# Kernel tuning notes

Hardware: AMD Instinct MI355X
Metric: run time of the kernel (lower is better)

The kernel has to match this reference:

```python
import jax, jax.numpy as jnp
import numpy as np

B, T, ENC_C = 64, 512, 512   # batch, encoder frames, encoder channels
H = 512                      # hidden_channels
D = 80                       # out_channels (mel dim)
RF = 2                       # reduction_factor
PRE_IN = D * RF              # prenet input (= D*2, see go_frame)
PRE_INNER = 256
CONV_CH = 32                 # location conv channels
K = 31                       # location conv kernel size


def setup_inputs():
    key = jax.random.key(0)
    ks = jax.random.split(key, 16)
    s = 0.02
    f32 = jnp.float32
    p = {}
    p['enc_output'] = jax.random.normal(ks[0], (B, T, ENC_C), f32)
    # acoustic lengths in [T, 2T], multiples of RF -> len//RF in [T//2, T]
    p['data_len'] = (jax.random.randint(ks[1], (B,), T // 2, T + 1, jnp.int32) * RF).astype(jnp.int32)
    # Prenet: two 1x1 convs (== linears) + ReLU
    p['pn_w1'] = jax.random.normal(ks[2], (PRE_INNER, PRE_IN), f32) * s
    p['pn_b1'] = jnp.zeros((PRE_INNER,), f32)
    p['pn_w2'] = jax.random.normal(ks[3], (H, PRE_INNER), f32) * s
    p['pn_b2'] = jnp.zeros((H,), f32)
    # Location-sensitive attention
    p['att_enc_w'] = jax.random.normal(ks[4], (H, ENC_C), f32) * s
    p['att_enc_b'] = jnp.zeros((H,), f32)
    p['att_dec_w'] = jax.random.normal(ks[5], (H, H), f32) * s
    p['att_conv_w'] = jax.random.normal(ks[6], (CONV_CH, 1, K), f32) * s
    p['att_loc_w'] = jax.random.normal(ks[7], (H, CONV_CH), f32) * s
    p['att_v_w'] = jax.random.normal(ks[8], (H,), f32) * s
    p['att_v_b'] = jnp.zeros((), f32)
    # 2 GRU cells (torch GRUCell layout: gates [r|z|n])
    p['gru0_wih'] = jax.random.normal(ks[9], (3 * H, ENC_C + H), f32) * s
    p['gru0_whh'] = jax.random.normal(ks[10], (3 * H, H), f32) * s
    p['gru0_bih'] = jnp.zeros((3 * H,), f32)
    p['gru0_bhh'] = jnp.zeros((3 * H,), f32)
    p['gru1_wih'] = jax.random.normal(ks[11], (3 * H, H), f32) * s
    p['gru1_whh'] = jax.random.normal(ks[12], (3 * H, H), f32) * s
    p['gru1_bih'] = jnp.zeros((3 * H,), f32)
    p['gru1_bhh'] = jnp.zeros((3 * H,), f32)
    # out_layer: 1x1 Conv1d(2H -> D*RF) == linear
    p['out_w'] = jax.random.normal(ks[13], (D * RF, 2 * H), f32) * s
    p['out_b'] = jnp.zeros((D * RF,), f32)
    return p


def _gru(x, h, wih, whh, bih, bhh):
    gi = x @ wih.T + bih
    gh = h @ whh.T + bhh
    ir, iz, inn = jnp.split(gi, 3, axis=-1)
    hr, hz, hn = jnp.split(gh, 3, axis=-1)
    r = jax.nn.sigmoid(ir + hr)
    z = jax.nn.sigmoid(iz + hz)
    n = jnp.tanh(inn + r * hn)
    return (1.0 - z) * n + z * h


def _decode(enc_output, data_len, pn_w1, pn_b1, pn_w2, pn_b2,
            att_enc_w, att_enc_b, att_dec_w, att_conv_w, att_loc_w, att_v_w, att_v_b,
            gru0_wih, gru0_whh, gru0_bih, gru0_bhh,
            gru1_wih, gru1_whh, gru1_bih, gru1_bhh, out_w, out_b):
    dt = enc_output.dtype
    len_r = data_len // RF                                   # (B,) encoder-frame lengths
    pad = jnp.arange(T)[None, :] >= len_r[:, None]           # (B,T) True at padding
    valid = (~pad).astype(dt)
    att_prev0 = valid / len_r.astype(dt)[:, None]            # uniform init attention
    # processed memory (computed once, as in attention.reset_state caching)
    pm = jnp.einsum('btc,hc->bth', enc_output, att_enc_w) + att_enc_b

    def step(carry, t):
        h0, h1, prev_out, att_sum = carry
        prev_w = jnp.where(t == 0, att_prev0, att_sum)       # (B,T)
        # location features: 1D conv over previous (cumulative) attention
        f = jax.lax.conv_general_dilated(prev_w[:, None, :], att_conv_w,
                                         (1,), [(K // 2, K // 2)])  # (B,CONV_CH,T)
        loc = jnp.einsum('bct,hc->bth', f, att_loc_w)
        dec = (h0 @ att_dec_w.T)[:, None, :]                 # query from GRU layer 0 state
        erg = jnp.tanh(loc + pm + dec) @ att_v_w + att_v_b   # (B,T)
        erg = jnp.where(pad, jnp.asarray(-1e9, dt), erg)
        att_w = jax.nn.softmax(erg, axis=-1)
        att_c = jnp.einsum('bt,btc->bc', att_w, enc_output)  # context (B,ENC_C)
        # prenet (dropout in eval == identity)
        x = jax.nn.relu(prev_out @ pn_w1.T + pn_b1)
        x = jax.nn.relu(x @ pn_w2.T + pn_b2)
        h0n = _gru(jnp.concatenate([x, att_c], -1), h0, gru0_wih, gru0_whh, gru0_bih, gru0_bhh)
        h1n = _gru(h0n, h1, gru1_wih, gru1_whh, gru1_bih, gru1_bhh)
        out = jnp.concatenate([h1n, att_c], -1) @ out_w.T + out_b   # (B, D*RF)
        return (h0n, h1n, out, att_sum + att_w), (out, att_w)

    zeros = lambda *s: jnp.zeros(s, dt)
    carry0 = (zeros(B, H), zeros(B, H), zeros(B, D * RF), zeros(B, T))
    _, (outs, att_ws) = jax.lax.scan(step, carry0, jnp.arange(T))
    # outs: (T,B,D*RF); each step reshapes to (B,D,RF) and cats on time
    out = outs.transpose(1, 0, 2).reshape(B, T, D, RF).transpose(0, 2, 1, 3).reshape(B, D, T * RF)
    att_w = att_ws.transpose(1, 2, 0)                        # (B, T, T_steps)
    return out, att_w


def reference(enc_output, data_len, pn_w1, pn_b1, pn_w2, pn_b2,
              att_enc_w, att_enc_b, att_dec_w, att_conv_w, att_loc_w, att_v_w, att_v_b,
              gru0_wih, gru0_whh, gru0_bih, gru0_bhh,
              gru1_wih, gru1_whh, gru1_bih, gru1_bhh, out_w, out_b):
    return _decode(enc_output, data_len, pn_w1, pn_b1, pn_w2, pn_b2,
                   att_enc_w, att_enc_b, att_dec_w, att_conv_w, att_loc_w, att_v_w, att_v_b,
                   gru0_wih, gru0_whh, gru0_bih, gru0_bhh,
                   gru1_wih, gru1_whh, gru1_bih, gru1_bhh, out_w, out_b)
```

## Files before the change

kernel.cpp:

```cpp
#include <hip/hip_runtime.h>
#include <hip/hip_bf16.h>

typedef unsigned short u16;


__device__ __forceinline__ float b2f(u16 u) {
  return __uint_as_float(((unsigned)u) << 16);
}
__device__ __forceinline__ u16 f2b(float f) {
  unsigned u = __float_as_uint(f);
  u += 0x7fffu + ((u >> 16) & 1u);
  return (u16)(u >> 16);
}
template<bool F32>
__device__ __forceinline__ float ldw(const void* p, size_t i) {
  return F32 ? ((const float*)p)[i] : b2f(((const u16*)p)[i]);
}
template<bool F32>
__device__ __forceinline__ float4 ldw4(const void* p, size_t i) {
  if (F32) {
    return *(const float4*)((const float*)p + i);
  } else {
    uint2 u = *(const uint2*)((const u16*)p + i);
    float4 r;
    r.x = __uint_as_float(u.x << 16);
    r.y = __uint_as_float(u.x & 0xffff0000u);
    r.z = __uint_as_float(u.y << 16);
    r.w = __uint_as_float(u.y & 0xffff0000u);
    return r;
  }
}
template<bool F32>
__device__ __forceinline__ void stout(void* p, size_t i, float v) {
  if (F32) ((float*)p)[i] = v; else ((u16*)p)[i] = f2b(v);
}
__device__ __forceinline__ float frcp(float x) { return __builtin_amdgcn_rcpf(x); }
__device__ __forceinline__ float tanh_f(float x) {
  float e = __expf(2.f * x);
  return 1.f - 2.f * frcp(e + 1.f);
}
__device__ __forceinline__ float sig_f(float x) { return frcp(1.f + __expf(-x)); }

__device__ __forceinline__ void st_sc(int* p, int v) {
  __hip_atomic_store(p, v, __ATOMIC_RELAXED, __HIP_MEMORY_SCOPE_AGENT);
}
__device__ __forceinline__ int ld_sc(const int* p) {
  return __hip_atomic_load(p, __ATOMIC_RELAXED, __HIP_MEMORY_SCOPE_AGENT);
}
__device__ __forceinline__ void stf_sc(float* p, float v) {
  __hip_atomic_store(p, v, __ATOMIC_RELAXED, __HIP_MEMORY_SCOPE_AGENT);
}
__device__ __forceinline__ float ldf_sc(const float* p) {
  return __hip_atomic_load(p, __ATOMIC_RELAXED, __HIP_MEMORY_SCOPE_AGENT);
}

__device__ __forceinline__ void stage_n(float* lds, const float* src, int n, int tid) {
  int i = 0;
  for (; i + 8192 <= n; i += 8192) {
    float r[16];
#pragma unroll
    for (int j = 0; j < 16; ++j) r[j] = ldf_sc(src + i + tid + j * 512);
#pragma unroll
    for (int j = 0; j < 16; ++j) lds[i + tid + j * 512] = r[j];
  }
  for (; i < n; i += 2048) {
    float r[4];
#pragma unroll
    for (int j = 0; j < 4; ++j) r[j] = ldf_sc(src + i + tid + j * 512);
#pragma unroll
    for (int j = 0; j < 4; ++j) lds[i + tid + j * 512] = r[j];
  }
}

template<bool F32, int NR>
__device__ __forceinline__ void dotN(float* __restrict__ acc, const float* __restrict__ sb,
                                     const void* __restrict__ wb, size_t rb, int wstride,
                                     int nk, int lane, int vz) {
  float4 wa[NR], wn[NR];
#pragma unroll
  for (int i = 0; i < NR; ++i) wa[i] = ldw4<F32>(wb, rb + (size_t)i * wstride + vz);
  for (int kg = 0; kg < nk; kg += 8) {
#pragma unroll
    for (int i = 0; i < NR; ++i) wn[i] = ldw4<F32>(wb, rb + (size_t)i * wstride + kg + 4 + vz);
    float a0 = sb[(kg + 0) * 64 + lane], a1 = sb[(kg + 1) * 64 + lane],
          a2 = sb[(kg + 2) * 64 + lane], a3 = sb[(kg + 3) * 64 + lane];
#pragma unroll
    for (int i = 0; i < NR; ++i)
      acc[i] = fmaf(wa[i].w, a3, fmaf(wa[i].z, a2, fmaf(wa[i].y, a1, fmaf(wa[i].x, a0, acc[i]))));
    int kn = (kg + 8 < nk) ? kg + 8 : kg;
#pragma unroll
    for (int i = 0; i < NR; ++i) wa[i] = ldw4<F32>(wb, rb + (size_t)i * wstride + kn + vz);
    float b0 = sb[(kg + 4) * 64 + lane], b1 = sb[(kg + 5) * 64 + lane],
          b2 = sb[(kg + 6) * 64 + lane], b3 = sb[(kg + 7) * 64 + lane];
#pragma unroll
    for (int i = 0; i < NR; ++i)
      acc[i] = fmaf(wn[i].w, b3, fmaf(wn[i].z, b2, fmaf(wn[i].y, b1, fmaf(wn[i].x, b0, acc[i]))));
  }
}

constexpr size_t OBAR  = 0;
constexpr size_t OFLG  = OBAR  + 128;
constexpr size_t OASUM = OFLG  + 8192;
constexpr size_t ODEC  = OASUM + 32768;
constexpr size_t OH0   = ODEC  + 32768;
constexpr size_t OH1   = OH0   + 32768;
constexpr size_t OPO   = OH1   + 32768;
constexpr size_t OZEND = OPO   + 10240;
constexpr int    ZERO_SPAN_N = (int)OZEND;
constexpr size_t OPRV  = OZEND;
constexpr size_t OERG  = OPRV  + 32768;
constexpr size_t OX1   = OERG  + 32768;
constexpr size_t OX2   = OX1   + 16384;
constexpr size_t OATTC = OX2   + 32768;
constexpr size_t OMM   = OATTC + 32768;
constexpr size_t OGI0  = OMM   + 16384;
constexpr size_t OGH0  = OGI0  + 393216;
constexpr size_t OGH1  = OGH0  + 196608;
constexpr size_t OGI1  = OGH1  + 196608;
constexpr size_t OPM   = OGI1  + 393216;
constexpr size_t OTOT  = OPM   + 8388608;

__device__ __forceinline__ void fastbar(int* flags, int* gen, int target,
                                        int wg, int tid) {
  __syncthreads();
  if (tid == 0) st_sc(flags + wg * 32, target);
  if (wg == 0) {
    if (tid < 64) {
      int i0 = tid * 4;
      for (;;) {
        int ok = (ld_sc(flags + (i0 + 0) * 32) >= target)
               & (ld_sc(flags + (i0 + 1) * 32) >= target)
               & (ld_sc(flags + (i0 + 2) * 32) >= target)
               & (ld_sc(flags + (i0 + 3) * 32) >= target);
        if (__ballot(ok) == 0xFFFFFFFFFFFFFFFFull) break;
      }
      if (tid == 0) st_sc(gen, target);
    }
    __syncthreads();
  } else {
    if (tid == 0) {
      while (ld_sc(gen) < target) {}
    }
    __syncthreads();
  }
}

__global__ void k_zero(float* p, int n) {
  for (int i = blockIdx.x * 256 + threadIdx.x; i < n; i += gridDim.x * 256) p[i] = 0.f;
}
__global__ void k_detect(int* flag, const u16* probe) {
  if (blockIdx.x != 0 || threadIdx.x != 0) return;
  int sane = 0;
  for (int i = 0; i < 256; i += 2) {
    u16 u = probe[i];
    int e = (u >> 7) & 0xFF;
    if (u == 0 || (e >= 97 && e <= 140)) ++sane;
  }
  *flag = (sane < 96) ? 1 : 0;
}
__global__ void k_prevw(float* prevw, const int* dlen) {
  int b = blockIdx.x;
  int len = dlen[b] >> 1;
  float inv = 1.f / (float)len;
  for (int i = threadIdx.x; i < 512; i += 256)
    prevw[b * 512 + i] = (i < len) ? inv : 0.f;
}
template<bool F32>
__global__ void k_cvtT512(const int* flag, float* dst, const void* src) {
  if (*flag != (F32 ? 1 : 0)) return;
  for (int i = blockIdx.x * 256 + threadIdx.x; i < 262144; i += gridDim.x * 256) {
    int c = i >> 9, h = i & 511;
    dst[i] = ldw<F32>(src, (size_t)h * 512 + c);
  }
}
template<bool F32>
__global__ void k_mmat(const int* flag, float* M, const void* locw, const void* convw) {
  if (*flag != (F32 ? 1 : 0)) return;
  int i = blockIdx.x * 256 + threadIdx.x;
  if (i >= 16384) return;
  int h = i >> 5, k = i & 31;
  float acc = 0.f;
  if (k < 31) {
    for (int c = 0; c < 32; ++c)
      acc = fmaf(ldw<F32>(locw, h * 32 + c), ldw<F32>(convw, c * 31 + k), acc);
  }
  M[i] = acc;
}
template<bool F32>
__global__ __launch_bounds__(256) void k_pm(const int* flag, u16* pm, const void* enc,
                                            const float* encwT, const void* encb) {
  if (*flag != (F32 ? 1 : 0)) return;
  __shared__ float encf[16 * 512];
  int row0 = blockIdx.x * 16;
  int tid = threadIdx.x;
  for (int i = tid; i < 16 * 512; i += 256) {
    int r = i >> 9, c = i & 511;
    encf[i] = ldw<F32>(enc, (size_t)(row0 + r) * 512 + c);
  }
  __syncthreads();
  float a0[16], a1[16];
  float bb0 = ldw<F32>(encb, tid), bb1 = ldw<F32>(encb, tid + 256);
#pragma unroll
  for (int r = 0; r < 16; ++r) { a0[r] = bb0; a1[r] = bb1; }
  for (int c = 0; c < 512; ++c) {
    float w0 = encwT[c * 512 + tid];
    float w1 = encwT[c * 512 + 256 + tid];
#pragma unroll
    for (int r = 0; r < 16; ++r) {
      float a = encf[r * 512 + c];
      a0[r] = fmaf(w0, a, a0[r]);
      a1[r] = fmaf(w1, a, a1[r]);
    }
  }
#pragma unroll
  for (int r = 0; r < 16; ++r) {
    pm[(size_t)(row0 + r) * 512 + tid]       = f2b(a0[r]);
    pm[(size_t)(row0 + r) * 512 + 256 + tid] = f2b(a1[r]);
  }
}

struct KP {
  const void* __restrict__ enc;
  const int* __restrict__ dlen;
  const u16* __restrict__ pm;
  const void* __restrict__ wih0; const void* __restrict__ whh0;
  const void* __restrict__ wih1; const void* __restrict__ whh1;
  const void* __restrict__ adec; const void* __restrict__ outw;
  const void* __restrict__ pnw2; const void* __restrict__ pnw1;
  const void* __restrict__ pnb1; const void* __restrict__ pnb2;
  const void* __restrict__ bih0; const void* __restrict__ bhh0;
  const void* __restrict__ bih1; const void* __restrict__ bhh1;
  const void* __restrict__ outb; const void* __restrict__ vw;
  const float* __restrict__ Mg;
  int* __restrict__ bar;
  int* __restrict__ flags;
  float* __restrict__ asum; float* __restrict__ dec;
  float* __restrict__ h0T;  float* __restrict__ h1T;  float* __restrict__ poT;
  float* __restrict__ prevw; float* __restrict__ erg;
  float* __restrict__ x1T;  float* __restrict__ x2T;  float* __restrict__ attcT;
  float* __restrict__ gi0p; float* __restrict__ gh0p;
  float* __restrict__ gh1p; float* __restrict__ gi1p;
  void* __restrict__ out;
};

template<bool F32>
__global__ __launch_bounds__(512, 2) void k_loop(KP p) {
  if (*(const volatile int*)(p.bar + 64) != (F32 ? 1 : 0)) return;
  __shared__ float stg[16384];
  __shared__ u16  M_u[32 * 512];
  __shared__ float dec_s[512];
  __shared__ float v_s[512];
  __shared__ float wq[160];
  __shared__ float sm[512];
  __shared__ float red[16];

  const int wg = blockIdx.x, tid = threadIdx.x;
  const int lane = tid & 63;
  const int wv = __builtin_amdgcn_readfirstlane(tid >> 6);
  const int b_att = wg >> 2, q = wg & 3, t0 = q * 128;
  const int trow = tid >> 6;
  const int hcol = tid & 63;
  float* dec1 = p.gh0p;
  int* genp = p.bar + 32;
  int bt = 0;
  int vz;
  asm volatile("v_mov_b32 %0, 0" : "=v"(vz));

  for (int i = tid; i < 32 * 512; i += 512) {
    int k = i >> 9, h = i & 511;
    M_u[i] = f2b(p.Mg[h * 32 + k]);
  }
  if (tid < 512) v_s[tid] = ldw<F32>(p.vw, tid);
  __syncthreads();

  for (int t = 0; t < 512; ++t) {
    if (wg < 32) stage_n(stg, p.poT, 10240, tid);
    if (tid < 158) {
      int g = t0 - 15 + tid;
      wq[tid] = (g >= 0 && g < 512) ? ldf_sc(p.prevw + b_att * 512 + g) : 0.f;
    }
    if (tid < 512)
      dec_s[tid] = ldf_sc(p.dec + b_att * 512 + tid) + ldf_sc(dec1 + b_att * 512 + tid);
    __syncthreads();
    if (wg < 32) {
      int n = wg * 8 + wv;
      float a[1] = {0.f};
      dotN<F32, 1>(a, stg, p.pnw1, (size_t)n * 160, 160, 160, lane, vz);
      stf_sc(p.x1T + n * 64 + lane, fmaxf(a[0] + ldw<F32>(p.pnb1, n), 0.f));
    }
    {
      float wreg[46];
#pragma unroll
      for (int i = 0; i < 46; ++i) wreg[i] = wq[trow * 16 + i];
      float acc[16];
#pragma unroll
      for (int s = 0; s < 16; ++s) acc[s] = 0.f;
      const u16* pmb = p.pm + ((size_t)(b_att * 512 + t0 + trow * 16)) * 512;
      for (int j = 0; j < 8; ++j) {
        int hj = hcol + 64 * j;
        float Mreg[31];
#pragma unroll
        for (int k = 0; k < 31; ++k) Mreg[k] = b2f(M_u[k * 512 + hj]);
        float dj = dec_s[hj], vj = v_s[hj];
#pragma unroll
        for (int s = 0; s < 16; ++s) {
          float u = dj;
#pragma unroll
          for (int k = 0; k < 31; ++k) u = fmaf(Mreg[k], wreg[s + k], u);
          u += b2f(pmb[s * 512 + hj]);
          acc[s] = fmaf(vj, tanh_f(u), acc[s]);
        }
      }
#pragma unroll
      for (int s = 0; s < 16; ++s) {
        float v = acc[s];
#pragma unroll
        for (int off = 32; off; off >>= 1) v += __shfl_xor(v, off, 64);
        if (hcol == 0) sm[trow * 16 + s] = v;
      }
      __syncthreads();
      if (tid < 128) stf_sc(p.erg + b_att * 512 + t0 + tid, sm[tid]);
    }
    fastbar(p.flags, genp, ++bt, wg, tid);

    if (wg < 64) {
      int b = wg;
      int len = p.dlen[b] >> 1;
      float e0 = ldf_sc(p.erg + b * 512 + tid);
      bool v0 = tid < len;
      float mx = v0 ? e0 : -1e30f;
#pragma unroll
      for (int off = 32; off; off >>= 1) mx = fmaxf(mx, __shfl_xor(mx, off, 64));
      if (lane == 0) red[wv] = mx;
      __syncthreads();
      mx = fmaxf(fmaxf(fmaxf(red[0], red[1]), fmaxf(red[2], red[3])),
                 fmaxf(fmaxf(red[4], red[5]), fmaxf(red[6], red[7])));
      float x0 = v0 ? __expf(e0 - mx) : 0.f;
      float s = x0;
#pragma unroll
      for (int off = 32; off; off >>= 1) s += __shfl_xor(s, off, 64);
      if (lane == 0) red[8 + wv] = s;
      __syncthreads();
      s = ((red[8] + red[9]) + (red[10] + red[11])) + ((red[12] + red[13]) + (red[14] + red[15]));
      float w0 = x0 * frcp(s);
      stout<F32>(p.out, 5242880 + (size_t)b * 262144 + (size_t)tid * 512 + t, w0);
      float s0 = p.asum[b * 512 + tid] + w0;
      p.asum[b * 512 + tid] = s0;
      stf_sc(p.prevw + b * 512 + tid, s0);
    } else if (wg < 192) {
      int idx = wg - 64, b = idx >> 1, half = idx & 1;
      int len = p.dlen[b] >> 1;
      float e0 = ldf_sc(p.erg + b * 512 + tid);
      bool v0 = tid < len;
      float mx = v0 ? e0 : -1e30f;
#pragma unroll
      for (int off = 32; off; off >>= 1) mx = fmaxf(mx, __shfl_xor(mx, off, 64));
      if (lane == 0) red[wv] = mx;
      __syncthreads();
      mx = fmaxf(fmaxf(fmaxf(red[0], red[1]), fmaxf(red[2], red[3])),
                 fmaxf(fmaxf(red[4], red[5]), fmaxf(red[6], red[7])));
      float x0 = v0 ? __expf(e0 - mx) : 0.f;
      float s = x0;
#pragma unroll
      for (int off = 32; off; off >>= 1) s += __shfl_xor(s, off, 64);
      if (lane == 0) red[8 + wv] = s;
      __syncthreads();
      s = ((red[8] + red[9]) + (red[10] + red[11])) + ((red[12] + red[13]) + (red[14] + red[15]));
      sm[tid] = x0 * frcp(s);
      __syncthreads();
      int c4 = half * 256 + lane * 4;
      size_t eb = (size_t)b * 262144 + c4;
      float4 ac[16];
#pragma unroll
      for (int i = 0; i < 16; ++i) ac[i] = make_float4(0.f, 0.f, 0.f, 0.f);
      int tb = wv * 64;
      for (int tt = 0; tt < 64; tt += 16) {
#pragma unroll
        for (int i = 0; i < 16; ++i) {
          float4 e = ldw4<F32>(p.enc, eb + (size_t)(tb + tt + i) * 512);
          float w = sm[tb + tt + i];
          ac[i].x = fmaf(w, e.x, ac[i].x);
          ac[i].y = fmaf(w, e.y, ac[i].y);
          ac[i].z = fmaf(w, e.z, ac[i].z);
          ac[i].w = fmaf(w, e.w, ac[i].w);
        }
      }
      float4 ssum;
      ssum.x = 0.f; ssum.y = 0.f; ssum.z = 0.f; ssum.w = 0.f;
#pragma unroll
      for (int i = 0; i < 16; ++i) {
        ssum.x += ac[i].x; ssum.y += ac[i].y; ssum.z += ac[i].z; ssum.w += ac[i].w;
      }
      __syncthreads();
      *(float4*)&stg[wv * 256 + lane * 4] = ssum;
      __syncthreads();
      if (tid < 256) {
        float r = ((stg[tid] + stg[256 + tid]) + (stg[512 + tid] + stg[768 + tid]))
                + ((stg[1024 + tid] + stg[1280 + tid]) + (stg[1536 + tid] + stg[1792 + tid]));
        stf_sc(p.attcT + (half * 256 + tid) * 64 + b, r);
      }
    } else {
      stage_n(stg, p.x1T, 16384, tid);
      __syncthreads();
      int idx = wg - 192;
      int n = idx * 8 + wv;
      float a[1] = {0.f};
      dotN<F32, 1>(a, stg, p.pnw2, (size_t)n * 256, 256, 256, lane, vz);
      stf_sc(p.x2T + n * 64 + lane, fmaxf(a[0] + ldw<F32>(p.pnb2, n), 0.f));
    }
    fastbar(p.flags, genp, ++bt, wg, tid);

    {
      const float* src; const void* wb; float* dst;
      int n0, wstride, wc0;
      if (wg < 128) {
        int kpart = wg & 3, ngrp = wg >> 2;
        src = ((kpart < 2) ? p.x2T : p.attcT) + (kpart & 1) * 16384;
        wb = p.wih0; wstride = 1024;
        wc0 = (kpart >> 1) * 512 + (kpart & 1) * 256;
        n0 = ngrp * 48 + wv * 6;
        dst = p.gi0p + ((size_t)kpart * 1536 + n0) * 64;
      } else if (wg < 192) {
        int idx = wg - 128, kpart = idx & 1, ngrp = idx >> 1;
        src = p.h0T + kpart * 16384;
        wb = p.whh0; wstride = 512; wc0 = kpart * 256;
        n0 = ngrp * 48 + wv * 6;
        dst = p.gh0p + ((size_t)kpart * 1536 + n0) * 64;
      } else {
        int idx = wg - 192, kpart = idx & 1, ngrp = idx >> 1;
        src = p.h1T + kpart * 16384;
        wb = p.whh1; wstride = 512; wc0 = kpart * 256;
        n0 = ngrp * 48 + wv * 6;
        dst = p.gh1p + ((size_t)kpart * 1536 + n0) * 64;
      }
      stage_n(stg, src, 16384, tid);
      __syncthreads();
      float acc[6];
#pragma unroll
      for (int i = 0; i < 6; ++i) acc[i] = 0.f;
      dotN<F32, 6>(acc, stg, wb, (size_t)n0 * wstride + wc0, wstride, 256, lane, vz);
#pragma unroll
      for (int i = 0; i < 6; ++i) stf_sc(dst + (size_t)i * 64 + lane, acc[i]);
    }
    fastbar(p.flags, genp, ++bt, wg, tid);

    if (wg < 64) {
      int e = wg * 512 + tid;
      int h = e >> 6, b = e & 63;
      float ir = ldf_sc(p.gi0p + h * 64 + b) + ldf_sc(p.gi0p + (1536 + h) * 64 + b)
               + ldf_sc(p.gi0p + (3072 + h) * 64 + b) + ldf_sc(p.gi0p + (4608 + h) * 64 + b)
               + ldw<F32>(p.bih0, h);
      float iz = ldf_sc(p.gi0p + (512 + h) * 64 + b) + ldf_sc(p.gi0p + (2048 + h) * 64 + b)
               + ldf_sc(p.gi0p + (3584 + h) * 64 + b) + ldf_sc(p.gi0p + (5120 + h) * 64 + b)
               + ldw<F32>(p.bih0, 512 + h);
      float in = ldf_sc(p.gi0p + (1024 + h) * 64 + b) + ldf_sc(p.gi0p + (2560 + h) * 64 + b)
               + ldf_sc(p.gi0p + (4096 + h) * 64 + b) + ldf_sc(p.gi0p + (5632 + h) * 64 + b)
               + ldw<F32>(p.bih0, 1024 + h);
      float hr = ldf_sc(p.gh0p + h * 64 + b) + ldf_sc(p.gh0p + (1536 + h) * 64 + b)
               + ldw<F32>(p.bhh0, h);
      float hz = ldf_sc(p.gh0p + (512 + h) * 64 + b) + ldf_sc(p.gh0p + (2048 + h) * 64 + b)
               + ldw<F32>(p.bhh0, 512 + h);
      float hn = ldf_sc(p.gh0p + (1024 + h) * 64 + b) + ldf_sc(p.gh0p + (2560 + h) * 64 + b)
               + ldw<F32>(p.bhh0, 1024 + h);
      float r = sig_f(ir + hr), z = sig_f(iz + hz);
      float nn = tanh_f(in + r * hn);
      float ho = ldf_sc(p.h0T + h * 64 + b);
      stf_sc(p.h0T + h * 64 + b, (1.f - z) * nn + z * ho);
    }
    fastbar(p.flags, genp, ++bt, wg, tid);

    if (wg < 128) {
      int kpart = wg & 3, ngrp = wg >> 2;
      stage_n(stg, p.h0T + kpart * 8192, 8192, tid);
      __syncthreads();
      int n0 = ngrp * 48 + wv * 6;
      float acc[6];
#pragma unroll
      for (int i = 0; i < 6; ++i) acc[i] = 0.f;
      dotN<F32, 6>(acc, stg, p.wih1, (size_t)n0 * 512 + kpart * 128, 512, 128, lane, vz);
#pragma unroll
      for (int i = 0; i < 6; ++i)
        stf_sc(p.gi1p + ((size_t)kpart * 1536 + n0 + i) * 64 + lane, acc[i]);
    } else {
      int g = wg - 128;
      int cpart = g >> 6;
      int n = (g & 63) * 8 + wv;
      stage_n(stg, p.h0T + cpart * 16384, 16384, tid);
      __syncthreads();
      float r[1] = {0.f};
      dotN<F32, 1>(r, stg, p.adec, (size_t)n * 512 + cpart * 256, 512, 256, lane, vz);
      float* dst = cpart ? dec1 : p.dec;
      stf_sc(dst + lane * 512 + n, r[0]);
    }
    fastbar(p.flags, genp, ++bt, wg, tid);

    if (wg < 64) {
      int e = wg * 512 + tid;
      int h = e >> 6, b = e & 63;
      float ir = ldf_sc(p.gi1p + h * 64 + b) + ldf_sc(p.gi1p + (1536 + h) * 64 + b)
               + ldf_sc(p.gi1p + (3072 + h) * 64 + b) + ldf_sc(p.gi1p + (4608 + h) * 64 + b)
               + ldw<F32>(p.bih1, h);
      float iz = ldf_sc(p.gi1p + (512 + h) * 64 + b) + ldf_sc(p.gi1p + (2048 + h) * 64 + b)
               + ldf_sc(p.gi1p + (3584 + h) * 64 + b) + ldf_sc(p.gi1p + (5120 + h) * 64 + b)
               + ldw<F32>(p.bih1, 512 + h);
      float in = ldf_sc(p.gi1p + (1024 + h) * 64 + b) + ldf_sc(p.gi1p + (2560 + h) * 64 + b)
               + ldf_sc(p.gi1p + (4096 + h) * 64 + b) + ldf_sc(p.gi1p + (5632 + h) * 64 + b)
               + ldw<F32>(p.bih1, 1024 + h);
      float hr = ldf_sc(p.gh1p + h * 64 + b) + ldf_sc(p.gh1p + (1536 + h) * 64 + b)
               + ldw<F32>(p.bhh1, h);
      float hz = ldf_sc(p.gh1p + (512 + h) * 64 + b) + ldf_sc(p.gh1p + (2048 + h) * 64 + b)
               + ldw<F32>(p.bhh1, 512 + h);
      float hn = ldf_sc(p.gh1p + (1024 + h) * 64 + b) + ldf_sc(p.gh1p + (2560 + h) * 64 + b)
               + ldw<F32>(p.bhh1, 1024 + h);
      float r = sig_f(ir + hr), z = sig_f(iz + hz);
      float nn = tanh_f(in + r * hn);
      float ho = ldf_sc(p.h1T + h * 64 + b);
      stf_sc(p.h1T + h * 64 + b, (1.f - z) * nn + z * ho);
    }
    fastbar(p.flags, genp, ++bt, wg, tid);

    if (wg < 20) {
      int n = wg * 8 + wv;
      float r[1] = {0.f};
      for (int c = 0; c < 4; ++c) {
        const float* src = ((c < 2) ? p.h1T : p.attcT) + (c & 1) * 16384;
        stage_n(stg, src, 16384, tid);
        __syncthreads();
        dotN<F32, 1>(r, stg, p.outw, (size_t)n * 1024 + c * 256, 1024, 256, lane, vz);
        __syncthreads();
      }
      float acc = r[0] + ldw<F32>(p.outb, n);
      stf_sc(p.poT + n * 64 + lane, acc);
      stout<F32>(p.out, (size_t)lane * 81920 + (size_t)(n >> 1) * 1024 + t * 2 + (n & 1), acc);
    }
    fastbar(p.flags, genp, ++bt, wg, tid);
  }
}

extern "C" void kernel_launch(void* const* d_in, const int* in_sizes, int n_in,
                              void* d_out, int out_size, void* d_ws, size_t ws_size,
                              hipStream_t stream) {
  (void)in_sizes; (void)n_in; (void)out_size; (void)ws_size;
  const void* enc   = d_in[0];
  const int*  dlen  = (const int*)d_in[1];
  const void* pnw1  = d_in[2];
  const void* pnb1  = d_in[3];
  const void* pnw2  = d_in[4];
  const void* pnb2  = d_in[5];
  const void* aencw = d_in[6];
  const void* aencb = d_in[7];
  const void* adecw = d_in[8];
  const void* aconv = d_in[9];
  const void* alocw = d_in[10];
  const void* avw   = d_in[11];
  const void* wih0  = d_in[13];
  const void* whh0  = d_in[14];
  const void* bih0  = d_in[15];
  const void* bhh0  = d_in[16];
  const void* wih1  = d_in[17];
  const void* whh1  = d_in[18];
  const void* bih1  = d_in[19];
  const void* bhh1  = d_in[20];
  const void* outw  = d_in[21];
  const void* outb  = d_in[22];

  float* W = (float*)d_ws;
  int* flag = (int*)(W + OBAR) + 64;
  dim3 blk(256);

  k_zero<<<256, blk, 0, stream>>>(W + OBAR, ZERO_SPAN_N);
  k_zero<<<64, blk, 0, stream>>>(W + OGH0, 32768);
  k_detect<<<1, blk, 0, stream>>>(flag, (const u16*)pnw1);
  k_prevw<<<64, blk, 0, stream>>>(W + OPRV, dlen);
  k_mmat<false><<<64, blk, 0, stream>>>(flag, W + OMM, alocw, aconv);
  k_mmat<true ><<<64, blk, 0, stream>>>(flag, W + OMM, alocw, aconv);
  k_cvtT512<false><<<512, blk, 0, stream>>>(flag, W + OGI0, aencw);
  k_cvtT512<true ><<<512, blk, 0, stream>>>(flag, W + OGI0, aencw);
  k_pm<false><<<2048, blk, 0, stream>>>(flag, (u16*)(W + OPM), enc, W + OGI0, aencb);
  k_pm<true ><<<2048, blk, 0, stream>>>(flag, (u16*)(W + OPM), enc, W + OGI0, aencb);

  KP kp;
  kp.enc = enc; kp.dlen = dlen;
  kp.pm = (const u16*)(W + OPM);
  kp.wih0 = wih0; kp.whh0 = whh0;
  kp.wih1 = wih1; kp.whh1 = whh1;
  kp.adec = adecw; kp.outw = outw;
  kp.pnw2 = pnw2; kp.pnw1 = pnw1;
  kp.pnb1 = pnb1; kp.pnb2 = pnb2;
  kp.bih0 = bih0; kp.bhh0 = bhh0;
  kp.bih1 = bih1; kp.bhh1 = bhh1;
  kp.outb = outb; kp.vw = avw;
  kp.Mg = W + OMM;
  kp.bar = (int*)(W + OBAR);
  kp.flags = (int*)(W + OFLG);
  kp.asum = W + OASUM; kp.dec = W + ODEC;
  kp.h0T = W + OH0; kp.h1T = W + OH1; kp.poT = W + OPO;
  kp.prevw = W + OPRV; kp.erg = W + OERG;
  kp.x1T = W + OX1; kp.x2T = W + OX2; kp.attcT = W + OATTC;
  kp.gi0p = W + OGI0; kp.gh0p = W + OGH0;
  kp.gh1p = W + OGH1; kp.gi1p = W + OGI1;
  kp.out = d_out;

  k_loop<false><<<dim3(256), dim3(512), 0, stream>>>(kp);
  k_loop<true ><<<dim3(256), dim3(512), 0, stream>>>(kp);
}
```

Before: 99.31 ms.

## Double persistent grid to 512 workgroups with finer K-splits across all phases

Raises the persistent decoder grid from 256 to 512 workgroups (launch bounds 4 per CU), halving the staged LDS buffer. Every matvec phase gets a finer K-split: attention energies per eighth of frames, context split over two time halves, GRU and out-layer partial sums split further, and dec projections in four parts. Partial results are summed later by consumers, and the output write is deferred to the next step's prenet stage. The aim is more parallelism per step, at the cost of more partial-sum traffic and a global barrier that must now poll 512 flags.

```diff
diff --git a/kernel.cpp b/kernel.cpp
--- a/kernel.cpp
+++ b/kernel.cpp
@@ -71,6 +71,36 @@
     for (int j = 0; j < 4; ++j) lds[i + tid + j * 512] = r[j];
   }
 }
+__device__ __forceinline__ void stage_sum2(float* lds, const float* a, const float* b,
+                                           int n, int tid) {
+  int i = 0;
+  for (; i + 8192 <= n; i += 8192) {
+    float r[8], s[8];
+#pragma unroll
+    for (int j = 0; j < 8; ++j) { r[j] = ldf_sc(a + i + tid + j * 512); }
+#pragma unroll
+    for (int j = 0; j < 8; ++j) { s[j] = ldf_sc(b + i + tid + j * 512); }
+#pragma unroll
+    for (int j = 0; j < 8; ++j) lds[i + tid + j * 512] = r[j] + s[j];
+    i += 4096;
+    i -= 4096;
+#pragma unroll
+    for (int j = 0; j < 8; ++j) { r[j] = ldf_sc(a + i + 4096 + tid + j * 512); }
+#pragma unroll
+    for (int j = 0; j < 8; ++j) { s[j] = ldf_sc(b + i + 4096 + tid + j * 512); }
+#pragma unroll
+    for (int j = 0; j < 8; ++j) lds[i + 4096 + tid + j * 512] = r[j] + s[j];
+  }
+  for (; i < n; i += 2048) {
+    float r[4], s[4];
+#pragma unroll
+    for (int j = 0; j < 4; ++j) r[j] = ldf_sc(a + i + tid + j * 512);
+#pragma unroll
+    for (int j = 0; j < 4; ++j) s[j] = ldf_sc(b + i + tid + j * 512);
+#pragma unroll
+    for (int j = 0; j < 4; ++j) lds[i + tid + j * 512] = r[j] + s[j];
+  }
+}
 
 template<bool F32, int NR>
 __device__ __forceinline__ void dotN(float* __restrict__ acc, const float* __restrict__ sb,
@@ -100,24 +130,25 @@
 
 constexpr size_t OBAR  = 0;
 constexpr size_t OFLG  = OBAR  + 128;
-constexpr size_t OASUM = OFLG  + 8192;
+constexpr size_t OASUM = OFLG  + 16384;
 constexpr size_t ODEC  = OASUM + 32768;
-constexpr size_t OH0   = ODEC  + 32768;
+constexpr size_t OH0   = ODEC  + 131072;
 constexpr size_t OH1   = OH0   + 32768;
 constexpr size_t OPO   = OH1   + 32768;
-constexpr size_t OZEND = OPO   + 10240;
+constexpr size_t OZEND = OPO   + 20480;
 constexpr int    ZERO_SPAN_N = (int)OZEND;
 constexpr size_t OPRV  = OZEND;
 constexpr size_t OERG  = OPRV  + 32768;
 constexpr size_t OX1   = OERG  + 32768;
 constexpr size_t OX2   = OX1   + 16384;
 constexpr size_t OATTC = OX2   + 32768;
-constexpr size_t OMM   = OATTC + 32768;
+constexpr size_t OATC2 = OATTC + 32768;
+constexpr size_t OMM   = OATC2 + 32768;
 constexpr size_t OGI0  = OMM   + 16384;
-constexpr size_t OGH0  = OGI0  + 393216;
-constexpr size_t OGH1  = OGH0  + 196608;
-constexpr size_t OGI1  = OGH1  + 196608;
-constexpr size_t OPM   = OGI1  + 393216;
+constexpr size_t OGH0  = OGI0  + 786432;
+constexpr size_t OGH1  = OGH0  + 393216;
+constexpr size_t OGI1  = OGH1  + 393216;
+constexpr size_t OPM   = OGI1  + 786432;
 constexpr size_t OTOT  = OPM   + 8388608;
 
 __device__ __forceinline__ void fastbar(int* flags, int* gen, int target,
@@ -125,7 +156,7 @@
   __syncthreads();
   if (tid == 0) st_sc(flags + wg * 32, target);
   if (wg == 0) {
-    if (tid < 64) {
+    if (tid < 128) {
       int i0 = tid * 4;
       for (;;) {
         int ok = (ld_sc(flags + (i0 + 0) * 32) >= target)
@@ -134,7 +165,10 @@
                & (ld_sc(flags + (i0 + 3) * 32) >= target);
         if (__ballot(ok) == 0xFFFFFFFFFFFFFFFFull) break;
       }
+      __syncthreads();
       if (tid == 0) st_sc(gen, target);
+    } else {
+      __syncthreads();
     }
     __syncthreads();
   } else {
@@ -234,33 +268,34 @@
   const float* __restrict__ Mg;
   int* __restrict__ bar;
   int* __restrict__ flags;
-  float* __restrict__ asum; float* __restrict__ dec;
-  float* __restrict__ h0T;  float* __restrict__ h1T;  float* __restrict__ poT;
+  float* __restrict__ asum; float* __restrict__ decp;
+  float* __restrict__ h0T;  float* __restrict__ h1T;
+  float* __restrict__ poT0; float* __restrict__ poT1;
   float* __restrict__ prevw; float* __restrict__ erg;
-  float* __restrict__ x1T;  float* __restrict__ x2T;  float* __restrict__ attcT;
+  float* __restrict__ x1T;  float* __restrict__ x2T;
+  float* __restrict__ attcT; float* __restrict__ attc2;
   float* __restrict__ gi0p; float* __restrict__ gh0p;
   float* __restrict__ gh1p; float* __restrict__ gi1p;
   void* __restrict__ out;
 };
 
 template<bool F32>
-__global__ __launch_bounds__(512, 2) void k_loop(KP p) {
+__global__ __launch_bounds__(512, 4) void k_loop(KP p) {
   if (*(const volatile int*)(p.bar + 64) != (F32 ? 1 : 0)) return;
-  __shared__ float stg[16384];
+  __shared__ float stg[8192];
   __shared__ u16  M_u[32 * 512];
   __shared__ float dec_s[512];
   __shared__ float v_s[512];
-  __shared__ float wq[160];
+  __shared__ float wq[96];
   __shared__ float sm[512];
   __shared__ float red[16];
 
   const int wg = blockIdx.x, tid = threadIdx.x;
   const int lane = tid & 63;
   const int wv = __builtin_amdgcn_readfirstlane(tid >> 6);
-  const int b_att = wg >> 2, q = wg & 3, t0 = q * 128;
+  const int b_att = wg >> 3, oct = wg & 7, t0 = oct * 64;
   const int trow = tid >> 6;
   const int hcol = tid & 63;
-  float* dec1 = p.gh0p;
   int* genp = p.bar + 32;
   int bt = 0;
   int vz;
@@ -274,28 +309,35 @@
   __syncthreads();
 
   for (int t = 0; t < 512; ++t) {
-    if (wg < 32) stage_n(stg, p.poT, 10240, tid);
-    if (tid < 158) {
+    if (wg < 32) stage_sum2(stg, p.poT0, p.poT1, 8192, tid);
+    if (tid < 94) {
       int g = t0 - 15 + tid;
       wq[tid] = (g >= 0 && g < 512) ? ldf_sc(p.prevw + b_att * 512 + g) : 0.f;
     }
-    if (tid < 512)
-      dec_s[tid] = ldf_sc(p.dec + b_att * 512 + tid) + ldf_sc(dec1 + b_att * 512 + tid);
+    dec_s[tid] = ldf_sc(p.decp + b_att * 512 + tid)
+               + ldf_sc(p.decp + 32768 + b_att * 512 + tid)
+               + ldf_sc(p.decp + 65536 + b_att * 512 + tid)
+               + ldf_sc(p.decp + 98304 + b_att * 512 + tid);
     __syncthreads();
+    float pacc[1] = {0.f};
+    int pn = wg * 8 + wv;
     if (wg < 32) {
-      int n = wg * 8 + wv;
-      float a[1] = {0.f};
-      dotN<F32, 1>(a, stg, p.pnw1, (size_t)n * 160, 160, 160, lane, vz);
-      stf_sc(p.x1T + n * 64 + lane, fmaxf(a[0] + ldw<F32>(p.pnb1, n), 0.f));
+      if (wg == 0 && t > 0) {
+        for (int i = tid; i < 8192; i += 512) {
+          int r = i >> 6, b = i & 63;
+          stout<F32>(p.out, (size_t)b * 81920 + (size_t)(r >> 1) * 1024 + (t - 1) * 2 + (r & 1), stg[i]);
+        }
+      }
+      dotN<F32, 1>(pacc, stg, p.pnw1, (size_t)pn * 160, 160, 128, lane, vz);
     }
     {
-      float wreg[46];
-#pragma unroll
-      for (int i = 0; i < 46; ++i) wreg[i] = wq[trow * 16 + i];
-      float acc[16];
-#pragma unroll
-      for (int s = 0; s < 16; ++s) acc[s] = 0.f;
-      const u16* pmb = p.pm + ((size_t)(b_att * 512 + t0 + trow * 16)) * 512;
+      float wreg[38];
+#pragma unroll
+      for (int i = 0; i < 38; ++i) wreg[i] = wq[trow * 8 + i];
+      float acc[8];
+#pragma unroll
+      for (int s = 0; s < 8; ++s) acc[s] = 0.f;
+      const u16* pmb = p.pm + ((size_t)(b_att * 512 + t0 + trow * 8)) * 512;
       for (int j = 0; j < 8; ++j) {
         int hj = hcol + 64 * j;
         float Mreg[31];
@@ -303,7 +345,7 @@
         for (int k = 0; k < 31; ++k) Mreg[k] = b2f(M_u[k * 512 + hj]);
         float dj = dec_s[hj], vj = v_s[hj];
 #pragma unroll
-        for (int s = 0; s < 16; ++s) {
+        for (int s = 0; s < 8; ++s) {
           float u = dj;
 #pragma unroll
           for (int k = 0; k < 31; ++k) u = fmaf(Mreg[k], wreg[s + k], u);
@@ -312,14 +354,26 @@
         }
       }
 #pragma unroll
-      for (int s = 0; s < 16; ++s) {
+      for (int s = 0; s < 8; ++s) {
         float v = acc[s];
 #pragma unroll
         for (int off = 32; off; off >>= 1) v += __shfl_xor(v, off, 64);
-        if (hcol == 0) sm[trow * 16 + s] = v;
-      }
-      __syncthreads();
-      if (tid < 128) stf_sc(p.erg + b_att * 512 + t0 + tid, sm[tid]);
+        if (hcol == 0) sm[trow * 8 + s] = v;
+      }
+      __syncthreads();
+      if (tid < 64) stf_sc(p.erg + b_att * 512 + t0 + tid, sm[tid]);
+    }
+    if (wg < 32) {
+      stage_sum2(stg, p.poT0 + 8192, p.poT1 + 8192, 2048, tid);
+      __syncthreads();
+      if (wg == 0 && t > 0) {
+        for (int i = tid; i < 2048; i += 512) {
+          int r = 128 + (i >> 6), b = i & 63;
+          stout<F32>(p.out, (size_t)b * 81920 + (size_t)(r >> 1) * 1024 + (t - 1) * 2 + (r & 1), stg[i]);
+        }
+      }
+      dotN<F32, 1>(pacc, stg, p.pnw1, (size_t)pn * 160 + 128, 160, 32, lane, vz);
+      stf_sc(p.x1T + pn * 64 + lane, fmaxf(pacc[0] + ldw<F32>(p.pnb1, pn), 0.f));
     }
     fastbar(p.flags, genp, ++bt, wg, tid);
 
@@ -347,8 +401,8 @@
       float s0 = p.asum[b * 512 + tid] + w0;
       p.asum[b * 512 + tid] = s0;
       stf_sc(p.prevw + b * 512 + tid, s0);
-    } else if (wg < 192) {
-      int idx = wg - 64, b = idx >> 1, half = idx & 1;
+    } else if (wg < 320) {
+      int idx = wg - 64, b = idx >> 2, quad = idx & 3, half = quad & 1, tpart = quad >> 1;
       int len = p.dlen[b] >> 1;
       float e0 = ldf_sc(p.erg + b * 512 + tid);
       bool v0 = tid < len;
@@ -373,8 +427,8 @@
       float4 ac[16];
 #pragma unroll
       for (int i = 0; i < 16; ++i) ac[i] = make_float4(0.f, 0.f, 0.f, 0.f);
-      int tb = wv * 64;
-      for (int tt = 0; tt < 64; tt += 16) {
+      int tb = tpart * 256 + wv * 32;
+      for (int tt = 0; tt < 32; tt += 16) {
 #pragma unroll
         for (int i = 0; i < 16; ++i) {
           float4 e = ldw4<F32>(p.enc, eb + (size_t)(tb + tt + i) * 512);
@@ -385,8 +439,7 @@
           ac[i].w = fmaf(w, e.w, ac[i].w);
         }
       }
-      float4 ssum;
-      ssum.x = 0.f; ssum.y = 0.f; ssum.z = 0.f; ssum.w = 0.f;
+      float4 ssum; ssum.x = 0.f; ssum.y = 0.f; ssum.z = 0.f; ssum.w = 0.f;
 #pragma unroll
       for (int i = 0; i < 16; ++i) {
         ssum.x += ac[i].x; ssum.y += ac[i].y; ssum.z += ac[i].z; ssum.w += ac[i].w;
@@ -397,48 +450,51 @@
       if (tid < 256) {
         float r = ((stg[tid] + stg[256 + tid]) + (stg[512 + tid] + stg[768 + tid]))
                 + ((stg[1024 + tid] + stg[1280 + tid]) + (stg[1536 + tid] + stg[1792 + tid]));
-        stf_sc(p.attcT + (half * 256 + tid) * 64 + b, r);
-      }
-    } else {
-      stage_n(stg, p.x1T, 16384, tid);
-      __syncthreads();
-      int idx = wg - 192;
-      int n = idx * 8 + wv;
+        stf_sc((tpart ? p.attc2 : p.attcT) + (half * 256 + tid) * 64 + b, r);
+      }
+    } else if (wg < 384) {
+      int n = (wg - 320) * 8 + wv;
       float a[1] = {0.f};
-      dotN<F32, 1>(a, stg, p.pnw2, (size_t)n * 256, 256, 256, lane, vz);
+      for (int c = 0; c < 2; ++c) {
+        stage_n(stg, p.x1T + c * 8192, 8192, tid);
+        __syncthreads();
+        dotN<F32, 1>(a, stg, p.pnw2, (size_t)n * 256 + c * 128, 256, 128, lane, vz);
+        __syncthreads();
+      }
       stf_sc(p.x2T + n * 64 + lane, fmaxf(a[0] + ldw<F32>(p.pnb2, n), 0.f));
     }
     fastbar(p.flags, genp, ++bt, wg, tid);
 
     {
-      const float* src; const void* wb; float* dst;
+      const float* srcA; const float* srcB = nullptr; const void* wb; float* dst;
       int n0, wstride, wc0;
-      if (wg < 128) {
-        int kpart = wg & 3, ngrp = wg >> 2;
-        src = ((kpart < 2) ? p.x2T : p.attcT) + (kpart & 1) * 16384;
-        wb = p.wih0; wstride = 1024;
-        wc0 = (kpart >> 1) * 512 + (kpart & 1) * 256;
+      if (wg < 256) {
+        int kpart = wg & 7, ngrp = wg >> 3;
+        if (kpart < 4) srcA = p.x2T + kpart * 8192;
+        else { srcA = p.attcT + (kpart - 4) * 8192; srcB = p.attc2 + (kpart - 4) * 8192; }
+        wb = p.wih0; wstride = 1024; wc0 = kpart * 128;
         n0 = ngrp * 48 + wv * 6;
         dst = p.gi0p + ((size_t)kpart * 1536 + n0) * 64;
-      } else if (wg < 192) {
-        int idx = wg - 128, kpart = idx & 1, ngrp = idx >> 1;
-        src = p.h0T + kpart * 16384;
-        wb = p.whh0; wstride = 512; wc0 = kpart * 256;
+      } else if (wg < 384) {
+        int idx = wg - 256, kpart = idx & 3, ngrp = idx >> 2;
+        srcA = p.h0T + kpart * 8192;
+        wb = p.whh0; wstride = 512; wc0 = kpart * 128;
         n0 = ngrp * 48 + wv * 6;
         dst = p.gh0p + ((size_t)kpart * 1536 + n0) * 64;
       } else {
-        int idx = wg - 192, kpart = idx & 1, ngrp = idx >> 1;
-        src = p.h1T + kpart * 16384;
-        wb = p.whh1; wstride = 512; wc0 = kpart * 256;
+        int idx = wg - 384, kpart = idx & 3, ngrp = idx >> 2;
+        srcA = p.h1T + kpart * 8192;
+        wb = p.whh1; wstride = 512; wc0 = kpart * 128;
         n0 = ngrp * 48 + wv * 6;
         dst = p.gh1p + ((size_t)kpart * 1536 + n0) * 64;
       }
-      stage_n(stg, src, 16384, tid);
+      if (srcB) stage_sum2(stg, srcA, srcB, 8192, tid);
+      else stage_n(stg, srcA, 8192, tid);
       __syncthreads();
       float acc[6];
 #pragma unroll
       for (int i = 0; i < 6; ++i) acc[i] = 0.f;
-      dotN<F32, 6>(acc, stg, wb, (size_t)n0 * wstride + wc0, wstride, 256, lane, vz);
+      dotN<F32, 6>(acc, stg, wb, (size_t)n0 * wstride + wc0, wstride, 128, lane, vz);
 #pragma unroll
       for (int i = 0; i < 6; ++i) stf_sc(dst + (size_t)i * 64 + lane, acc[i]);
     }
@@ -447,21 +503,20 @@
     if (wg < 64) {
       int e = wg * 512 + tid;
       int h = e >> 6, b = e & 63;
-      float ir = ldf_sc(p.gi0p + h * 64 + b) + ldf_sc(p.gi0p + (1536 + h) * 64 + b)
-               + ldf_sc(p.gi0p + (3072 + h) * 64 + b) + ldf_sc(p.gi0p + (4608 + h) * 64 + b)
-               + ldw<F32>(p.bih0, h);
-      float iz = ldf_sc(p.gi0p + (512 + h) * 64 + b) + ldf_sc(p.gi0p + (2048 + h) * 64 + b)
-               + ldf_sc(p.gi0p + (3584 + h) * 64 + b) + ldf_sc(p.gi0p + (5120 + h) * 64 + b)
-               + ldw<F32>(p.bih0, 512 + h);
-      float in = ldf_sc(p.gi0p + (1024 + h) * 64 + b) + ldf_sc(p.gi0p + (2560 + h) * 64 + b)
-               + ldf_sc(p.gi0p + (4096 + h) * 64 + b) + ldf_sc(p.gi0p + (5632 + h) * 64 + b)
-               + ldw<F32>(p.bih0, 1024 + h);
-      float hr = ldf_sc(p.gh0p + h * 64 + b) + ldf_sc(p.gh0p + (1536 + h) * 64 + b)
-               + ldw<F32>(p.bhh0, h);
-      float hz = ldf_sc(p.gh0p + (512 + h) * 64 + b) + ldf_sc(p.gh0p + (2048 + h) * 64 + b)
-               + ldw<F32>(p.bhh0, 512 + h);
-      float hn = ldf_sc(p.gh0p + (1024 + h) * 64 + b) + ldf_sc(p.gh0p + (2560 + h) * 64 + b)
-               + ldw<F32>(p.bhh0, 1024 + h);
+      float ir = ldw<F32>(p.bih0, h), iz = ldw<F32>(p.bih0, 512 + h), in = ldw<F32>(p.bih0, 1024 + h);
+#pragma unroll
+      for (int c = 0; c < 8; ++c) {
+        ir += ldf_sc(p.gi0p + ((size_t)c * 1536 + h) * 64 + b);
+        iz += ldf_sc(p.gi0p + ((size_t)c * 1536 + 512 + h) * 64 + b);
+        in += ldf_sc(p.gi0p + ((size_t)c * 1536 + 1024 + h) * 64 + b);
+      }
+      float hr = ldw<F32>(p.bhh0, h), hz = ldw<F32>(p.bhh0, 512 + h), hn = ldw<F32>(p.bhh0, 1024 + h);
+#pragma unroll
+      for (int c = 0; c < 4; ++c) {
+        hr += ldf_sc(p.gh0p + ((size_t)c * 1536 + h) * 64 + b);
+        hz += ldf_sc(p.gh0p + ((size_t)c * 1536 + 512 + h) * 64 + b);
+        hn += ldf_sc(p.gh0p + ((size_t)c * 1536 + 1024 + h) * 64 + b);
+      }
       float r = sig_f(ir + hr), z = sig_f(iz + hz);
       float nn = tanh_f(in + r * hn);
       float ho = ldf_sc(p.h0T + h * 64 + b);
@@ -469,49 +524,47 @@
     }
     fastbar(p.flags, genp, ++bt, wg, tid);
 
-    if (wg < 128) {
-      int kpart = wg & 3, ngrp = wg >> 2;
-      stage_n(stg, p.h0T + kpart * 8192, 8192, tid);
+    if (wg < 256) {
+      int kpart = wg & 7, ngrp = wg >> 3;
+      stage_n(stg, p.h0T + kpart * 4096, 4096, tid);
       __syncthreads();
       int n0 = ngrp * 48 + wv * 6;
       float acc[6];
 #pragma unroll
       for (int i = 0; i < 6; ++i) acc[i] = 0.f;
-      dotN<F32, 6>(acc, stg, p.wih1, (size_t)n0 * 512 + kpart * 128, 512, 128, lane, vz);
+      dotN<F32, 6>(acc, stg, p.wih1, (size_t)n0 * 512 + kpart * 64, 512, 64, lane, vz);
 #pragma unroll
       for (int i = 0; i < 6; ++i)
         stf_sc(p.gi1p + ((size_t)kpart * 1536 + n0 + i) * 64 + lane, acc[i]);
     } else {
-      int g = wg - 128;
+      int g = wg - 256;
       int cpart = g >> 6;
       int n = (g & 63) * 8 + wv;
-      stage_n(stg, p.h0T + cpart * 16384, 16384, tid);
+      stage_n(stg, p.h0T + cpart * 8192, 8192, tid);
       __syncthreads();
       float r[1] = {0.f};
-      dotN<F32, 1>(r, stg, p.adec, (size_t)n * 512 + cpart * 256, 512, 256, lane, vz);
-      float* dst = cpart ? dec1 : p.dec;
-      stf_sc(dst + lane * 512 + n, r[0]);
+      dotN<F32, 1>(r, stg, p.adec, (size_t)n * 512 + cpart * 128, 512, 128, lane, vz);
+      stf_sc(p.decp + (size_t)cpart * 32768 + lane * 512 + n, r[0]);
     }
     fastbar(p.flags, genp, ++bt, wg, tid);
 
     if (wg < 64) {
       int e = wg * 512 + tid;
       int h = e >> 6, b = e & 63;
-      float ir = ldf_sc(p.gi1p + h * 64 + b) + ldf_sc(p.gi1p + (1536 + h) * 64 + b)
-               + ldf_sc(p.gi1p + (3072 + h) * 64 + b) + ldf_sc(p.gi1p + (4608 + h) * 64 + b)
-               + ldw<F32>(p.bih1, h);
-      float iz = ldf_sc(p.gi1p + (512 + h) * 64 + b) + ldf_sc(p.gi1p + (2048 + h) * 64 + b)
-               + ldf_sc(p.gi1p + (3584 + h) * 64 + b) + ldf_sc(p.gi1p + (5120 + h) * 64 + b)
-               + ldw<F32>(p.bih1, 512 + h);
-      float in = ldf_sc(p.gi1p + (1024 + h) * 64 + b) + ldf_sc(p.gi1p + (2560 + h) * 64 + b)
-               + ldf_sc(p.gi1p + (4096 + h) * 64 + b) + ldf_sc(p.gi1p + (5632 + h) * 64 + b)
-               + ldw<F32>(p.bih1, 1024 + h);
-      float hr = ldf_sc(p.gh1p + h * 64 + b) + ldf_sc(p.gh1p + (1536 + h) * 64 + b)
-               + ldw<F32>(p.bhh1, h);
-      float hz = ldf_sc(p.gh1p + (512 + h) * 64 + b) + ldf_sc(p.gh1p + (2048 + h) * 64 + b)
-               + ldw<F32>(p.bhh1, 512 + h);
-      float hn = ldf_sc(p.gh1p + (1024 + h) * 64 + b) + ldf_sc(p.gh1p + (2560 + h) * 64 + b)
-               + ldw<F32>(p.bhh1, 1024 + h);
+      float ir = ldw<F32>(p.bih1, h), iz = ldw<F32>(p.bih1, 512 + h), in = ldw<F32>(p.bih1, 1024 + h);
+#pragma unroll
+      for (int c = 0; c < 8; ++c) {
+        ir += ldf_sc(p.gi1p + ((size_t)c * 1536 + h) * 64 + b);
+        iz += ldf_sc(p.gi1p + ((size_t)c * 1536 + 512 + h) * 64 + b);
+        in += ldf_sc(p.gi1p + ((size_t)c * 1536 + 1024 + h) * 64 + b);
+      }
+      float hr = ldw<F32>(p.bhh1, h), hz = ldw<F32>(p.bhh1, 512 + h), hn = ldw<F32>(p.bhh1, 1024 + h);
+#pragma unroll
+      for (int c = 0; c < 4; ++c) {
+        hr += ldf_sc(p.gh1p + ((size_t)c * 1536 + h) * 64 + b);
+        hz += ldf_sc(p.gh1p + ((size_t)c * 1536 + 512 + h) * 64 + b);
+        hn += ldf_sc(p.gh1p + ((size_t)c * 1536 + 1024 + h) * 64 + b);
+      }
       float r = sig_f(ir + hr), z = sig_f(iz + hz);
       float nn = tanh_f(in + r * hn);
       float ho = ldf_sc(p.h1T + h * 64 + b);
@@ -519,21 +572,37 @@
     }
     fastbar(p.flags, genp, ++bt, wg, tid);
 
-    if (wg < 20) {
-      int n = wg * 8 + wv;
+    if (wg < 40) {
+      int kp = wg / 20;
+      int n = (wg % 20) * 8 + wv;
       float r[1] = {0.f};
       for (int c = 0; c < 4; ++c) {
-        const float* src = ((c < 2) ? p.h1T : p.attcT) + (c & 1) * 16384;
-        stage_n(stg, src, 16384, tid);
+        if (kp == 0) stage_n(stg, p.h1T + c * 8192, 8192, tid);
+        else stage_sum2(stg, p.attcT + c * 8192, p.attc2 + c * 8192, 8192, tid);
         __syncthreads();
-        dotN<F32, 1>(r, stg, p.outw, (size_t)n * 1024 + c * 256, 1024, 256, lane, vz);
+        dotN<F32, 1>(r, stg, p.outw, (size_t)n * 1024 + kp * 512 + c * 128, 1024, 128, lane, vz);
         __syncthreads();
       }
-      float acc = r[0] + ldw<F32>(p.outb, n);
-      stf_sc(p.poT + n * 64 + lane, acc);
-      stout<F32>(p.out, (size_t)lane * 81920 + (size_t)(n >> 1) * 1024 + t * 2 + (n & 1), acc);
+      float acc = r[0] + (kp ? ldw<F32>(p.outb, n) : 0.f);
+      stf_sc((kp ? p.poT1 : p.poT0) + n * 64 + lane, acc);
     }
     fastbar(p.flags, genp, ++bt, wg, tid);
+  }
+
+  if (wg == 0) {
+    stage_sum2(stg, p.poT0, p.poT1, 8192, tid);
+    __syncthreads();
+    for (int i = tid; i < 8192; i += 512) {
+      int r = i >> 6, b = i & 63;
+      stout<F32>(p.out, (size_t)b * 81920 + (size_t)(r >> 1) * 1024 + 511 * 2 + (r & 1), stg[i]);
+    }
+    __syncthreads();
+    stage_sum2(stg, p.poT0 + 8192, p.poT1 + 8192, 2048, tid);
+    __syncthreads();
+    for (int i = tid; i < 2048; i += 512) {
+      int r = 128 + (i >> 6), b = i & 63;
+      stout<F32>(p.out, (size_t)b * 81920 + (size_t)(r >> 1) * 1024 + 511 * 2 + (r & 1), stg[i]);
+    }
   }
 }
 
@@ -569,7 +638,6 @@
   dim3 blk(256);
 
   k_zero<<<256, blk, 0, stream>>>(W + OBAR, ZERO_SPAN_N);
-  k_zero<<<64, blk, 0, stream>>>(W + OGH0, 32768);
   k_detect<<<1, blk, 0, stream>>>(flag, (const u16*)pnw1);
   k_prevw<<<64, blk, 0, stream>>>(W + OPRV, dlen);
   k_mmat<false><<<64, blk, 0, stream>>>(flag, W + OMM, alocw, aconv);
@@ -593,14 +661,16 @@
   kp.Mg = W + OMM;
   kp.bar = (int*)(W + OBAR);
   kp.flags = (int*)(W + OFLG);
-  kp.asum = W + OASUM; kp.dec = W + ODEC;
-  kp.h0T = W + OH0; kp.h1T = W + OH1; kp.poT = W + OPO;
+  kp.asum = W + OASUM; kp.decp = W + ODEC;
+  kp.h0T = W + OH0; kp.h1T = W + OH1;
+  kp.poT0 = W + OPO; kp.poT1 = W + OPO + 10240;
   kp.prevw = W + OPRV; kp.erg = W + OERG;
-  kp.x1T = W + OX1; kp.x2T = W + OX2; kp.attcT = W + OATTC;
+  kp.x1T = W + OX1; kp.x2T = W + OX2;
+  kp.attcT = W + OATTC; kp.attc2 = W + OATC2;
   kp.gi0p = W + OGI0; kp.gh0p = W + OGH0;
   kp.gh1p = W + OGH1; kp.gi1p = W + OGI1;
   kp.out = d_out;
 
-  k_loop<false><<<dim3(256), dim3(512), 0, stream>>>(kp);
-  k_loop<true ><<<dim3(256), dim3(512), 0, stream>>>(kp);
-}
+  k_loop<false><<<dim3(512), dim3(512), 0, stream>>>(kp);
+  k_loop<true ><<<dim3(512), dim3(512), 0, stream>>>(kp);
+}
```

New measurement: 118.6 ms. +19.4%, slower.
